# Kernel optimization log

Hardware: AMD Instinct MI355X
Metric: run time of the kernel (lower is better)

Reference implementation:

```python
import jax, jax.numpy as jnp
import numpy as np

N, E = 50000, 800000
IN_C, HID = 128, 256


def _lin_params(key, fan_in, fan_out, bias=True):
    k1, k2 = jax.random.split(key)
    bound = 1.0 / np.sqrt(fan_in)
    W = jax.random.uniform(k1, (fan_in, fan_out), minval=-bound, maxval=bound, dtype=jnp.float32)
    if bias:
        b = jax.random.uniform(k2, (fan_out,), minval=-bound, maxval=bound, dtype=jnp.float32)
        return W, b
    return W


def setup_inputs() -> dict:
    key = jax.random.key(0)
    ks = jax.random.split(key, 8)
    x = jax.random.normal(ks[0], (N, IN_C), dtype=jnp.float32)
    edge_index = jax.random.randint(ks[1], (2, E), 0, N, dtype=jnp.int64)
    Wl0, bl0 = _lin_params(ks[2], IN_C, HID)
    Wr0 = _lin_params(ks[3], IN_C, HID, bias=False)
    Wl1, bl1 = _lin_params(ks[4], HID, HID)
    Wr1 = _lin_params(ks[5], HID, HID, bias=False)
    Wl2, bl2 = _lin_params(ks[6], HID, HID)
    Wr2 = _lin_params(ks[7], HID, HID, bias=False)
    return {"x": x, "edge_index": edge_index,
            "Wl0": Wl0, "bl0": bl0, "Wr0": Wr0,
            "Wl1": Wl1, "bl1": bl1, "Wr1": Wr1,
            "Wl2": Wl2, "bl2": bl2, "Wr2": Wr2}


def reference(x, edge_index, Wl0, bl0, Wr0, Wl1, bl1, Wr1, Wl2, bl2, Wr2):
    # PyG SAGEConv (mean aggr): out = lin_l(mean_{j in N(i)} x_j) + lin_r(x_i)
    src, dst = edge_index[0], edge_index[1]
    n = x.shape[0]
    deg = jax.ops.segment_sum(jnp.ones((src.shape[0],), jnp.float32), dst, num_segments=n)
    inv_deg = jnp.where(deg > 0, 1.0 / jnp.maximum(deg, 1.0), 0.0)[:, None]

    def sage_layer(h, Wl, bl, Wr):
        agg = jax.ops.segment_sum(h[src], dst, num_segments=n) * inv_deg  # mean over in-neighbors
        return jax.nn.relu(agg @ Wl + bl + h @ Wr)  # dropout is a no-op at inference

    h = sage_layer(x, Wl0, bl0, Wr0)
    h = sage_layer(h, Wl1, bl1, Wr1)
    h = sage_layer(h, Wl2, bl2, Wr2)
    return h
```

## Files before the change

### kernel.cpp

```cpp
#include <hip/hip_runtime.h>
#include <cstdint>
#include <cstddef>


typedef __bf16 bf16x8 __attribute__((ext_vector_type(8)));
typedef __bf16 bf16x4 __attribute__((ext_vector_type(4)));
typedef float  f32x4  __attribute__((ext_vector_type(4)));

static inline size_t align_up(size_t x, size_t a) { return (x + a - 1) / a * a; }

__device__ __forceinline__ void gload_lds16(const void* g, void* l) {
    __builtin_amdgcn_global_load_lds(
        (const __attribute__((address_space(1))) void*)g,
        (__attribute__((address_space(3))) void*)l, 16, 0, 0);
}

__global__ void deg_kernel(const int* __restrict__ dst, int* __restrict__ deg, int E) {
    int i = blockIdx.x * blockDim.x + threadIdx.x;
    if (i < E) atomicAdd(&deg[dst[i]], 1);
}

__global__ void scan_a(const int* __restrict__ deg, int* __restrict__ blocksums, int n) {
    __shared__ int ts[256];
    int t = threadIdx.x;
    int base = blockIdx.x * 1024 + t * 4;
    int s = 0;
    #pragma unroll
    for (int j = 0; j < 4; ++j) if (base + j < n) s += deg[base + j];
    ts[t] = s;
    __syncthreads();
    #pragma unroll
    for (int off = 128; off >= 1; off >>= 1) {
        if (t < off) ts[t] += ts[t + off];
        __syncthreads();
    }
    if (t == 0) blocksums[blockIdx.x] = ts[0];
}

__global__ void scan_b(const int* __restrict__ blocksums, int* __restrict__ blockoff,
                       int NB, int* __restrict__ rowptr_n) {
    __shared__ int ts[256];
    int t = threadIdx.x;
    int v = (t < NB) ? blocksums[t] : 0;
    ts[t] = v;
    __syncthreads();
    for (int off = 1; off < 256; off <<= 1) {
        int u = (t >= off) ? ts[t - off] : 0;
        __syncthreads();
        ts[t] += u;
        __syncthreads();
    }
    if (t < NB) blockoff[t] = ts[t] - v;
    if (t == 255) *rowptr_n = ts[255];
}

__global__ void scan_c(const int* __restrict__ deg, const int* __restrict__ blockoff,
                       int* __restrict__ rowptr, int* __restrict__ cursor,
                       float* __restrict__ inv_deg, int n) {
    __shared__ int ts[256];
    int t = threadIdx.x;
    int base = blockIdx.x * 1024 + t * 4;
    int d[4];
    int s = 0;
    #pragma unroll
    for (int j = 0; j < 4; ++j) {
        d[j] = (base + j < n) ? deg[base + j] : 0;
        s += d[j];
    }
    ts[t] = s;
    __syncthreads();
    for (int off = 1; off < 256; off <<= 1) {
        int u = (t >= off) ? ts[t - off] : 0;
        __syncthreads();
        ts[t] += u;
        __syncthreads();
    }
    int ex = ts[t] - s + blockoff[blockIdx.x];
    #pragma unroll
    for (int j = 0; j < 4; ++j) {
        if (base + j < n) {
            rowptr[base + j] = ex;
            cursor[base + j] = ex;
            inv_deg[base + j] = d[j] > 0 ? 1.0f / (float)d[j] : 0.0f;
            ex += d[j];
        }
    }
}

__global__ void fill_kernel(const int* __restrict__ src, const int* __restrict__ dst,
                            int* __restrict__ cursor, int* __restrict__ csr, int E) {
    int i = blockIdx.x * blockDim.x + threadIdx.x;
    if (i < E) {
        int p = atomicAdd(&cursor[dst[i]], 1);
        csr[p] = src[i];
    }
}

__global__ void f32_to_bf16(const float* __restrict__ in, uint16_t* __restrict__ out, int count) {
    int i = (blockIdx.x * blockDim.x + threadIdx.x) * 8;
    if (i >= count) return;
    float4 v0 = *(const float4*)(in + i);
    float4 v1 = *(const float4*)(in + i + 4);
    bf16x8 o;
    o[0] = (__bf16)v0.x; o[1] = (__bf16)v0.y; o[2] = (__bf16)v0.z; o[3] = (__bf16)v0.w;
    o[4] = (__bf16)v1.x; o[5] = (__bf16)v1.y; o[6] = (__bf16)v1.z; o[7] = (__bf16)v1.w;
    *(bf16x8*)(out + i) = o;
}

__device__ inline void addq(float* a, uint32_t u0, uint32_t u1, uint32_t u2, uint32_t u3) {
    uint32_t u[4] = {u0, u1, u2, u3};
    #pragma unroll
    for (int i = 0; i < 4; ++i) {
        a[2 * i]     += __uint_as_float(u[i] << 16);
        a[2 * i + 1] += __uint_as_float(u[i] & 0xffff0000u);
    }
}

template<int C>
__global__ void agg_bf16(const uint16_t* __restrict__ hb, const int* __restrict__ rowptr,
                         const int* __restrict__ csr, const float* __restrict__ inv_deg,
                         uint16_t* __restrict__ aggb, int n) {
    constexpr int LPN = C / 8;
    constexpr int NPB = 256 / LPN;
    int node = blockIdx.x * NPB + (int)(threadIdx.x / LPN);
    if (node >= n) return;
    int sub = threadIdx.x % LPN;
    int b = rowptr[node], e = rowptr[node + 1];
    float acc[8] = {0.f, 0.f, 0.f, 0.f, 0.f, 0.f, 0.f, 0.f};
    const uint4* h4 = (const uint4*)hb;
    int k = b;
    for (; k + 3 < e; k += 4) {
        int s0 = csr[k], s1 = csr[k + 1], s2 = csr[k + 2], s3 = csr[k + 3];
        uint4 q0 = h4[(size_t)s0 * LPN + sub];
        uint4 q1 = h4[(size_t)s1 * LPN + sub];
        uint4 q2 = h4[(size_t)s2 * LPN + sub];
        uint4 q3 = h4[(size_t)s3 * LPN + sub];
        addq(acc, q0.x, q0.y, q0.z, q0.w);
        addq(acc, q1.x, q1.y, q1.z, q1.w);
        addq(acc, q2.x, q2.y, q2.z, q2.w);
        addq(acc, q3.x, q3.y, q3.z, q3.w);
    }
    for (; k < e; ++k) {
        uint4 q = h4[(size_t)csr[k] * LPN + sub];
        addq(acc, q.x, q.y, q.z, q.w);
    }
    float id = inv_deg[node];
    bf16x8 o;
    #pragma unroll
    for (int j = 0; j < 8; ++j) o[j] = (__bf16)(acc[j] * id);
    *(bf16x8*)(aggb + (size_t)node * C + sub * 8) = o;
}

__global__ void convert_w(const float* __restrict__ Wl, const float* __restrict__ Wr,
                          uint8_t* __restrict__ Wpre, int K1) {
    int c = threadIdx.x;
    int kbase = blockIdx.x * 4;
    bf16x4 hi4;
    #pragma unroll
    for (int j = 0; j < 4; ++j) {
        int k = kbase + j;
        float w = (k < K1) ? Wl[(size_t)k * 256 + c] : Wr[(size_t)(k - K1) * 256 + c];
        hi4[j] = (__bf16)w;
    }
    int s = kbase >> 5;
    int kk = kbase & 31;
    int lane = (c & 15) + ((kk >> 3) << 4);
    uint32_t byte = (uint32_t)(c >> 4) * 1024 + (uint32_t)lane * 16 + (uint32_t)(kk & 7) * 2;
    *(bf16x4*)(Wpre + (size_t)s * 16384 + byte) = hi4;
}

__device__ inline uint16_t f2bf(float f) {
    __bf16 h = (__bf16)f;
    union { __bf16 b; uint16_t u; } c;
    c.b = h;
    return c.u;
}

template<int K1>
__global__ __launch_bounds__(256, 3)
void gemm_mfma(const uint16_t* __restrict__ A1, const uint16_t* __restrict__ A2,
               const uint8_t* __restrict__ Wpre, const float* __restrict__ bias,
               float* __restrict__ out, uint16_t* __restrict__ outb, int n) {
    constexpr int S1 = K1 / 32;
    constexpr int NT = 2 * S1;
    __shared__ __align__(16) uint8_t ldsA[2][8192];
    __shared__ __align__(16) uint8_t ldsW[2][8192];

    const int tid = threadIdx.x;
    const int l = tid & 63;
    const int w = tid >> 6;
    const int lr = l & 15;
    const int lg = l >> 4;
    const int row0 = (blockIdx.x >> 1) * 128;
    const int cb = blockIdx.x & 1;
    const int wr = w & 1;
    const int cw = w >> 1;

    f32x4 acc[4][4];
    #pragma unroll
    for (int mt = 0; mt < 4; ++mt)
        #pragma unroll
        for (int nt = 0; nt < 4; ++nt)
            acc[mt][nt] = (f32x4)(0.f);

    const int key = (lr >> 1) & 3;
    uint32_t abyte[4];
    #pragma unroll
    for (int mt = 0; mt < 4; ++mt)
        abyte[mt] = (uint32_t)((wr * 64 + mt * 16 + lr) * 64 + ((lg ^ key) << 4));
    uint32_t wrbyte[4];
    #pragma unroll
    for (int nt = 0; nt < 4; ++nt)
        wrbyte[nt] = (uint32_t)((cw * 4 + nt) * 1024 + l * 16);

    auto stage = [&](int s, int buf) {
        const uint16_t* __restrict__ A = (s < S1) ? A1 : A2;
        int kl = ((s < S1) ? s : s - S1) * 32;
        #pragma unroll
        for (int i = 0; i < 2; ++i) {
            int b = w * 2 + i;
            int r = b * 16 + (l >> 2);
            int kq = (l & 3) ^ ((r >> 1) & 3);
            gload_lds16(A + (size_t)(row0 + r) * K1 + kl + kq * 8,
                        &ldsA[buf][b * 1024]);
        }
        const uint8_t* __restrict__ Ws = Wpre + (size_t)s * 16384 + (size_t)cb * 8192;
        #pragma unroll
        for (int i = 0; i < 2; ++i) {
            int b = w * 2 + i;
            gload_lds16(Ws + b * 1024 + l * 16, &ldsW[buf][b * 1024]);
        }
    };

    auto domfma = [&](int buf) {
        bf16x8 bh[4];
        #pragma unroll
        for (int nt = 0; nt < 4; ++nt)
            bh[nt] = *(const bf16x8*)(&ldsW[buf][wrbyte[nt]]);
        #pragma unroll
        for (int mt = 0; mt < 4; ++mt) {
            bf16x8 a = *(const bf16x8*)(&ldsA[buf][abyte[mt]]);
            #pragma unroll
            for (int nt = 0; nt < 4; ++nt)
                acc[mt][nt] = __builtin_amdgcn_mfma_f32_16x16x32_bf16(a, bh[nt], acc[mt][nt], 0, 0, 0);
        }
    };

    stage(0, 0);
    __syncthreads();
    #pragma unroll 1
    for (int s = 0; s < NT; ++s) {
        int buf = s & 1;
        if (s + 1 < NT) stage(s + 1, buf ^ 1);
        domfma(buf);
        __syncthreads();
    }

    #pragma unroll
    for (int nt = 0; nt < 4; ++nt) {
        int col = cb * 128 + cw * 64 + nt * 16 + lr;
        float bv = bias[col];
        #pragma unroll
        for (int mt = 0; mt < 4; ++mt) {
            #pragma unroll
            for (int rr = 0; rr < 4; ++rr) {
                int grow = row0 + wr * 64 + mt * 16 + lg * 4 + rr;
                if (grow < n) {
                    float v = fmaxf(acc[mt][nt][rr] + bv, 0.f);
                    if (out)  out[(size_t)grow * 256 + col] = v;
                    if (outb) outb[(size_t)grow * 256 + col] = f2bf(v);
                }
            }
        }
    }
}

extern "C" void kernel_launch(void* const* d_in, const int* in_sizes, int n_in,
                              void* d_out, int out_size, void* d_ws, size_t ws_size,
                              hipStream_t stream) {
    const float* x   = (const float*)d_in[0];
    const int* edge  = (const int*)d_in[1];
    const float* Wl0 = (const float*)d_in[2];
    const float* bl0 = (const float*)d_in[3];
    const float* Wr0 = (const float*)d_in[4];
    const float* Wl1 = (const float*)d_in[5];
    const float* bl1 = (const float*)d_in[6];
    const float* Wr1 = (const float*)d_in[7];
    const float* Wl2 = (const float*)d_in[8];
    const float* bl2 = (const float*)d_in[9];
    const float* Wr2 = (const float*)d_in[10];

    int n = in_sizes[0] / 128;
    int E = in_sizes[1] / 2;
    int npad = n + 128;
    const int* src = edge;
    const int* dst = edge + E;

    char* wptr = (char*)d_ws;
    auto alloc = [&](size_t bytes) { char* p = wptr; wptr += align_up(bytes, 256); return p; };
    int*      deg    = (int*)alloc((size_t)n * 4);
    int*      rowptr = (int*)alloc(((size_t)n + 1) * 4);
    int*      cursor = (int*)alloc((size_t)n * 4);
    int*      csr    = (int*)alloc((size_t)E * 4);
    float*    invd   = (float*)alloc((size_t)n * 4);
    int*      bsums  = (int*)alloc(256 * 4);
    int*      boff   = (int*)alloc(256 * 4);
    uint8_t*  Wp0    = (uint8_t*)alloc(8 * 16384);
    uint8_t*  Wp1    = (uint8_t*)alloc(16 * 16384);
    uint8_t*  Wp2    = (uint8_t*)alloc(16 * 16384);
    uint16_t* xb     = (uint16_t*)alloc((size_t)npad * 128 * 2);
    uint16_t* aggb   = (uint16_t*)alloc((size_t)npad * 256 * 2);
    uint16_t* h0b    = (uint16_t*)alloc((size_t)npad * 256 * 2);
    uint16_t* h1b    = (uint16_t*)alloc((size_t)npad * 256 * 2);

    int NB = (n + 1023) / 1024;
    hipMemsetAsync(deg, 0, (size_t)n * 4, stream);
    deg_kernel<<<(E + 255) / 256, 256, 0, stream>>>(dst, deg, E);
    scan_a<<<NB, 256, 0, stream>>>(deg, bsums, n);
    scan_b<<<1, 256, 0, stream>>>(bsums, boff, NB, rowptr + n);
    scan_c<<<NB, 256, 0, stream>>>(deg, boff, rowptr, cursor, invd, n);
    fill_kernel<<<(E + 255) / 256, 256, 0, stream>>>(src, dst, cursor, csr, E);

    convert_w<<<2 * 128 / 4, 256, 0, stream>>>(Wl0, Wr0, Wp0, 128);
    convert_w<<<2 * 256 / 4, 256, 0, stream>>>(Wl1, Wr1, Wp1, 256);
    convert_w<<<2 * 256 / 4, 256, 0, stream>>>(Wl2, Wr2, Wp2, 256);

    int cx = n * 128;
    f32_to_bf16<<<(cx / 8 + 255) / 256, 256, 0, stream>>>(x, xb, cx);

    int gemm_grid = ((n + 127) / 128) * 2;
    agg_bf16<128><<<(n + 15) / 16, 256, 0, stream>>>(xb, rowptr, csr, invd, aggb, n);
    gemm_mfma<128><<<gemm_grid, 256, 0, stream>>>(aggb, xb, Wp0, bl0, (float*)nullptr, h0b, n);
    agg_bf16<256><<<(n + 7) / 8, 256, 0, stream>>>(h0b, rowptr, csr, invd, aggb, n);
    gemm_mfma<256><<<gemm_grid, 256, 0, stream>>>(aggb, h0b, Wp1, bl1, (float*)nullptr, h1b, n);
    agg_bf16<256><<<(n + 7) / 8, 256, 0, stream>>>(h1b, rowptr, csr, invd, aggb, n);
    gemm_mfma<256><<<gemm_grid, 256, 0, stream>>>(aggb, h1b, Wp2, bl2, (float*)d_out, (uint16_t*)nullptr, n);
}
```

Before: 349.7 us.

## Triple-buffer GEMM LDS staging with partial vmcnt waits; merge weight-convert launches

The MFMA GEMM moves from double to triple-buffered LDS staging. Tile s+2 is prefetched while tile s is computed, and there is one barrier per step gated by a partial s_waitcnt vmcnt instead of a full drain plus __syncthreads. The aim is to keep more global-to-LDS loads in flight and cut stall time at barriers. This raises LDS use to 48KB per block, which may lower occupancy under launch_bounds(256,3). Separately, the three convert_w launches are merged into one to save launch overhead.

```diff
diff --git a/kernel.cpp b/kernel.cpp
--- a/kernel.cpp
+++ b/kernel.cpp
@@ -151,10 +151,20 @@
     *(bf16x8*)(aggb + (size_t)node * C + sub * 8) = o;
 }
 
-__global__ void convert_w(const float* __restrict__ Wl, const float* __restrict__ Wr,
-                          uint8_t* __restrict__ Wpre, int K1) {
+__global__ void convert_w_all(const float* __restrict__ Wl0, const float* __restrict__ Wr0,
+                              uint8_t* __restrict__ Wp0,
+                              const float* __restrict__ Wl1, const float* __restrict__ Wr1,
+                              uint8_t* __restrict__ Wp1,
+                              const float* __restrict__ Wl2, const float* __restrict__ Wr2,
+                              uint8_t* __restrict__ Wp2) {
+    int bid = blockIdx.x;
+    const float *Wl, *Wr;
+    uint8_t* Wpre;
+    int K1, kbase;
+    if (bid < 64)       { Wl = Wl0; Wr = Wr0; Wpre = Wp0; K1 = 128; kbase = bid * 4; }
+    else if (bid < 192) { Wl = Wl1; Wr = Wr1; Wpre = Wp1; K1 = 256; kbase = (bid - 64) * 4; }
+    else                { Wl = Wl2; Wr = Wr2; Wpre = Wp2; K1 = 256; kbase = (bid - 192) * 4; }
     int c = threadIdx.x;
-    int kbase = blockIdx.x * 4;
     bf16x4 hi4;
     #pragma unroll
     for (int j = 0; j < 4; ++j) {
@@ -183,8 +193,8 @@
                float* __restrict__ out, uint16_t* __restrict__ outb, int n) {
     constexpr int S1 = K1 / 32;
     constexpr int NT = 2 * S1;
-    __shared__ __align__(16) uint8_t ldsA[2][8192];
-    __shared__ __align__(16) uint8_t ldsW[2][8192];
+    __shared__ __align__(16) uint8_t ldsA[3][8192];
+    __shared__ __align__(16) uint8_t ldsW[3][8192];
 
     const int tid = threadIdx.x;
     const int l = tid & 63;
@@ -247,14 +257,21 @@
     };
 
     stage(0, 0);
-    __syncthreads();
+    stage(1, 1);
     #pragma unroll 1
-    for (int s = 0; s < NT; ++s) {
-        int buf = s & 1;
-        if (s + 1 < NT) stage(s + 1, buf ^ 1);
-        domfma(buf);
-        __syncthreads();
-    }
+    for (int s = 0; s < NT - 1; ++s) {
+        asm volatile("s_waitcnt vmcnt(4)" ::: "memory");
+        __builtin_amdgcn_sched_barrier(0);
+        __builtin_amdgcn_s_barrier();
+        __builtin_amdgcn_sched_barrier(0);
+        if (s + 2 < NT) stage(s + 2, (s + 2) % 3);
+        domfma(s % 3);
+    }
+    asm volatile("s_waitcnt vmcnt(0)" ::: "memory");
+    __builtin_amdgcn_sched_barrier(0);
+    __builtin_amdgcn_s_barrier();
+    __builtin_amdgcn_sched_barrier(0);
+    domfma((NT - 1) % 3);
 
     #pragma unroll
     for (int nt = 0; nt < 4; ++nt) {
@@ -321,9 +338,7 @@
     scan_c<<<NB, 256, 0, stream>>>(deg, boff, rowptr, cursor, invd, n);
     fill_kernel<<<(E + 255) / 256, 256, 0, stream>>>(src, dst, cursor, csr, E);
 
-    convert_w<<<2 * 128 / 4, 256, 0, stream>>>(Wl0, Wr0, Wp0, 128);
-    convert_w<<<2 * 256 / 4, 256, 0, stream>>>(Wl1, Wr1, Wp1, 256);
-    convert_w<<<2 * 256 / 4, 256, 0, stream>>>(Wl2, Wr2, Wp2, 256);
+    convert_w_all<<<320, 256, 0, stream>>>(Wl0, Wr0, Wp0, Wl1, Wr1, Wp1, Wl2, Wr2, Wp2);
 
     int cx = n * 128;
     f32_to_bf16<<<(cx / 8 + 255) / 256, 256, 0, stream>>>(x, xb, cx);
```

After: 378.1 us. 1.08x slower.

## Narrow GEMM tiles to 64 columns with K=64 stages and merge weight conversion

Applied to the files above, without the earlier changes.

The GEMM block tile shrinks from 128x128 to 128x64 output columns, which doubles the grid, and each pipeline stage now covers K=64 (two 32-wide substeps) instead of K=32, halving the number of barriers and stages. Each A tile is now loaded four times (once per column quarter) instead of twice, and LDS per block grows to 48KB. The accumulator array is halved, which may raise occupancy. The three weight-conversion launches are also merged into a single kernel to cut launch overhead.

```diff
diff --git a/kernel.cpp b/kernel.cpp
--- a/kernel.cpp
+++ b/kernel.cpp
@@ -151,10 +151,20 @@
     *(bf16x8*)(aggb + (size_t)node * C + sub * 8) = o;
 }
 
-__global__ void convert_w(const float* __restrict__ Wl, const float* __restrict__ Wr,
-                          uint8_t* __restrict__ Wpre, int K1) {
+__global__ void convert_w_all(const float* __restrict__ Wl0, const float* __restrict__ Wr0,
+                              uint8_t* __restrict__ Wp0,
+                              const float* __restrict__ Wl1, const float* __restrict__ Wr1,
+                              uint8_t* __restrict__ Wp1,
+                              const float* __restrict__ Wl2, const float* __restrict__ Wr2,
+                              uint8_t* __restrict__ Wp2) {
+    int bid = blockIdx.x;
+    const float *Wl, *Wr;
+    uint8_t* Wpre;
+    int K1, kbase;
+    if (bid < 64)       { Wl = Wl0; Wr = Wr0; Wpre = Wp0; K1 = 128; kbase = bid * 4; }
+    else if (bid < 192) { Wl = Wl1; Wr = Wr1; Wpre = Wp1; K1 = 256; kbase = (bid - 64) * 4; }
+    else                { Wl = Wl2; Wr = Wr2; Wpre = Wp2; K1 = 256; kbase = (bid - 192) * 4; }
     int c = threadIdx.x;
-    int kbase = blockIdx.x * 4;
     bf16x4 hi4;
     #pragma unroll
     for (int j = 0; j < 4; ++j) {
@@ -181,9 +191,9 @@
 void gemm_mfma(const uint16_t* __restrict__ A1, const uint16_t* __restrict__ A2,
                const uint8_t* __restrict__ Wpre, const float* __restrict__ bias,
                float* __restrict__ out, uint16_t* __restrict__ outb, int n) {
-    constexpr int S1 = K1 / 32;
-    constexpr int NT = 2 * S1;
-    __shared__ __align__(16) uint8_t ldsA[2][8192];
+    constexpr int NT = K1 / 32;
+    constexpr int SH = K1 / 64;
+    __shared__ __align__(16) uint8_t ldsA[2][16384];
     __shared__ __align__(16) uint8_t ldsW[2][8192];
 
     const int tid = threadIdx.x;
@@ -191,16 +201,16 @@
     const int w = tid >> 6;
     const int lr = l & 15;
     const int lg = l >> 4;
-    const int row0 = (blockIdx.x >> 1) * 128;
-    const int cb = blockIdx.x & 1;
+    const int row0 = (blockIdx.x >> 2) * 128;
+    const int cq = blockIdx.x & 3;
     const int wr = w & 1;
     const int cw = w >> 1;
 
-    f32x4 acc[4][4];
+    f32x4 acc[4][2];
     #pragma unroll
     for (int mt = 0; mt < 4; ++mt)
         #pragma unroll
-        for (int nt = 0; nt < 4; ++nt)
+        for (int nt = 0; nt < 2; ++nt)
             acc[mt][nt] = (f32x4)(0.f);
 
     const int key = (lr >> 1) & 3;
@@ -208,41 +218,49 @@
     #pragma unroll
     for (int mt = 0; mt < 4; ++mt)
         abyte[mt] = (uint32_t)((wr * 64 + mt * 16 + lr) * 64 + ((lg ^ key) << 4));
-    uint32_t wrbyte[4];
-    #pragma unroll
-    for (int nt = 0; nt < 4; ++nt)
-        wrbyte[nt] = (uint32_t)((cw * 4 + nt) * 1024 + l * 16);
+    uint32_t wrbyte[2];
+    #pragma unroll
+    for (int nt = 0; nt < 2; ++nt)
+        wrbyte[nt] = (uint32_t)((cw * 2 + nt) * 1024 + l * 16);
 
     auto stage = [&](int s, int buf) {
-        const uint16_t* __restrict__ A = (s < S1) ? A1 : A2;
-        int kl = ((s < S1) ? s : s - S1) * 32;
+        const uint16_t* __restrict__ A = (s < SH) ? A1 : A2;
+        int kl = ((s < SH) ? s : s - SH) * 64;
+        #pragma unroll
+        for (int i = 0; i < 4; ++i) {
+            int b = w * 4 + i;
+            int kk = b >> 3;
+            int rg = b & 7;
+            int r = rg * 16 + (l >> 2);
+            int kq = (l & 3) ^ ((r >> 1) & 3);
+            gload_lds16(A + (size_t)(row0 + r) * K1 + kl + kk * 32 + kq * 8,
+                        &ldsA[buf][b * 1024]);
+        }
         #pragma unroll
         for (int i = 0; i < 2; ++i) {
             int b = w * 2 + i;
-            int r = b * 16 + (l >> 2);
-            int kq = (l & 3) ^ ((r >> 1) & 3);
-            gload_lds16(A + (size_t)(row0 + r) * K1 + kl + kq * 8,
-                        &ldsA[buf][b * 1024]);
-        }
-        const uint8_t* __restrict__ Ws = Wpre + (size_t)s * 16384 + (size_t)cb * 8192;
-        #pragma unroll
-        for (int i = 0; i < 2; ++i) {
-            int b = w * 2 + i;
-            gload_lds16(Ws + b * 1024 + l * 16, &ldsW[buf][b * 1024]);
+            int kk = b >> 2;
+            int cgl = b & 3;
+            const uint8_t* src = Wpre + (size_t)(s * 2 + kk) * 16384
+                               + (size_t)cq * 4096 + (size_t)cgl * 1024 + (size_t)l * 16;
+            gload_lds16(src, &ldsW[buf][b * 1024]);
         }
     };
 
     auto domfma = [&](int buf) {
-        bf16x8 bh[4];
-        #pragma unroll
-        for (int nt = 0; nt < 4; ++nt)
-            bh[nt] = *(const bf16x8*)(&ldsW[buf][wrbyte[nt]]);
-        #pragma unroll
-        for (int mt = 0; mt < 4; ++mt) {
-            bf16x8 a = *(const bf16x8*)(&ldsA[buf][abyte[mt]]);
+        #pragma unroll
+        for (int kk = 0; kk < 2; ++kk) {
+            bf16x8 bh[2];
             #pragma unroll
-            for (int nt = 0; nt < 4; ++nt)
-                acc[mt][nt] = __builtin_amdgcn_mfma_f32_16x16x32_bf16(a, bh[nt], acc[mt][nt], 0, 0, 0);
+            for (int nt = 0; nt < 2; ++nt)
+                bh[nt] = *(const bf16x8*)(&ldsW[buf][kk * 4096 + wrbyte[nt]]);
+            #pragma unroll
+            for (int mt = 0; mt < 4; ++mt) {
+                bf16x8 a = *(const bf16x8*)(&ldsA[buf][kk * 8192 + abyte[mt]]);
+                #pragma unroll
+                for (int nt = 0; nt < 2; ++nt)
+                    acc[mt][nt] = __builtin_amdgcn_mfma_f32_16x16x32_bf16(a, bh[nt], acc[mt][nt], 0, 0, 0);
+            }
         }
     };
 
@@ -257,8 +275,8 @@
     }
 
     #pragma unroll
-    for (int nt = 0; nt < 4; ++nt) {
-        int col = cb * 128 + cw * 64 + nt * 16 + lr;
+    for (int nt = 0; nt < 2; ++nt) {
+        int col = cq * 64 + cw * 32 + nt * 16 + lr;
         float bv = bias[col];
         #pragma unroll
         for (int mt = 0; mt < 4; ++mt) {
@@ -321,14 +339,12 @@
     scan_c<<<NB, 256, 0, stream>>>(deg, boff, rowptr, cursor, invd, n);
     fill_kernel<<<(E + 255) / 256, 256, 0, stream>>>(src, dst, cursor, csr, E);
 
-    convert_w<<<2 * 128 / 4, 256, 0, stream>>>(Wl0, Wr0, Wp0, 128);
-    convert_w<<<2 * 256 / 4, 256, 0, stream>>>(Wl1, Wr1, Wp1, 256);
-    convert_w<<<2 * 256 / 4, 256, 0, stream>>>(Wl2, Wr2, Wp2, 256);
+    convert_w_all<<<320, 256, 0, stream>>>(Wl0, Wr0, Wp0, Wl1, Wr1, Wp1, Wl2, Wr2, Wp2);
 
     int cx = n * 128;
     f32_to_bf16<<<(cx / 8 + 255) / 256, 256, 0, stream>>>(x, xb, cx);
 
-    int gemm_grid = ((n + 127) / 128) * 2;
+    int gemm_grid = ((n + 127) / 128) * 4;
     agg_bf16<128><<<(n + 15) / 16, 256, 0, stream>>>(xb, rowptr, csr, invd, aggb, n);
     gemm_mfma<128><<<gemm_grid, 256, 0, stream>>>(aggb, xb, Wp0, bl0, (float*)nullptr, h0b, n);
     agg_bf16<256><<<(n + 7) / 8, 256, 0, stream>>>(h0b, rowptr, csr, invd, aggb, n);
```

Result: slower. 387.5 us (+10.8%).
